# Optimization experiments

Measured on AMD Instinct MI355X. Metric: run time of the kernel, lower is better.

## Reference

```python
import jax, jax.numpy as jnp
import numpy as np

B, H, W, DIM, WS, SHIFT, HEADS = 32, 56, 56, 256, 7, 3, 8
N = WS * WS          # 49 tokens per window
C2 = 2 * DIM         # concatenated two-modal channel dim
NW = (H // WS) * (W // WS)


def _rel_index(ws):
    coords = np.stack(np.meshgrid(np.arange(ws), np.arange(ws), indexing='ij')).reshape(2, -1)
    rel = (coords[:, :, None] - coords[:, None, :]).transpose(1, 2, 0)
    rel[:, :, 0] += ws - 1
    rel[:, :, 1] += ws - 1
    rel[:, :, 0] *= 2 * ws - 1
    return rel.sum(-1)  # (N, N) int

REL_IDX = _rel_index(WS).reshape(-1)


def _attn_mask():
    # standard Swin shifted-window mask: 0 / -100 per window pair
    img = np.zeros((H, W))
    cnt = 0
    for hs in (slice(0, H - WS), slice(H - WS, H - SHIFT), slice(H - SHIFT, H)):
        for ws_ in (slice(0, W - WS), slice(W - WS, W - SHIFT), slice(W - SHIFT, W)):
            img[hs, ws_] = cnt
            cnt += 1
    mw = img.reshape(H // WS, WS, W // WS, WS).transpose(0, 2, 1, 3).reshape(-1, N)
    d = mw[:, None, :] - mw[:, :, None]
    return np.where(d != 0, -100.0, 0.0).astype(np.float32)  # (nW, N, N)

ATTN_MASK = _attn_mask()


def _win_part(x):  # (B,H,W,C) -> (nW*B, N, C)
    b, c = x.shape[0], x.shape[-1]
    x = x.reshape(b, H // WS, WS, W // WS, WS, c).transpose(0, 1, 3, 2, 4, 5)
    return x.reshape(-1, N, c)


def _win_rev(w, b):  # (nW*B, N, C) -> (B,H,W,C)
    c = w.shape[-1]
    x = w.reshape(b, H // WS, W // WS, WS, WS, c).transpose(0, 1, 3, 2, 4, 5)
    return x.reshape(b, H, W, c)


def _ln(t, g, bb):
    m = t.mean(-1, keepdims=True)
    v = t.var(-1, keepdims=True)
    return (t - m) / jnp.sqrt(v + 1e-5) * g + bb


def setup_inputs() -> dict:
    key = jax.random.key(0)
    ks = jax.random.split(key, 8)
    def nrm(k, shape, s=0.02):
        return jax.random.normal(k, shape, jnp.float32) * s
    return {
        'x': jax.random.normal(ks[0], (B, H * W, DIM), jnp.float32),
        'y': jax.random.normal(ks[1], (B, H * W, DIM), jnp.float32),
        'g1': jnp.ones((DIM,), jnp.float32), 'b1': jnp.zeros((DIM,), jnp.float32),
        'rpb': nrm(ks[2], ((2 * WS - 1) * (2 * WS - 1), HEADS)),
        'w_qkv': nrm(ks[3], (6 * DIM, 2 * DIM)), 'b_qkv': jnp.zeros((6 * DIM,), jnp.float32),
        'w_proj': nrm(ks[4], (DIM, 2 * DIM)), 'b_proj': jnp.zeros((DIM,), jnp.float32),
        'g2': jnp.ones((DIM,), jnp.float32), 'b2': jnp.zeros((DIM,), jnp.float32),
        'w_fc1': nrm(ks[5], (4 * DIM, DIM)), 'b_fc1': jnp.zeros((4 * DIM,), jnp.float32),
        'w_fc2': nrm(ks[6], (DIM, 4 * DIM)), 'b_fc2': jnp.zeros((DIM,), jnp.float32),
    }


def reference(x, y, g1, b1, rpb, w_qkv, b_qkv, w_proj, b_proj, g2, b2, w_fc1, b_fc1, w_fc2, b_fc2):
    scale = (DIM // HEADS) ** -0.5  # as in __init__: head_dim = dim // num_heads
    shortcut = x
    xn = _ln(x, g1, b1).reshape(B, H, W, DIM)
    yn = _ln(y, g1, b1).reshape(B, H, W, DIM)
    # cyclic shift
    xn = jnp.roll(xn, (-SHIFT, -SHIFT), axis=(1, 2))
    yn = jnp.roll(yn, (-SHIFT, -SHIFT), axis=(1, 2))
    xw, yw = _win_part(xn), _win_part(yn)            # (nW*B, N, C)
    xy = jnp.concatenate([xw, yw], axis=-1)          # (nW*B, N, 2C)
    nwb, hd = xy.shape[0], C2 // HEADS
    qkv = (xy @ w_qkv.T + b_qkv).reshape(nwb, N, 3, HEADS, hd).transpose(2, 0, 3, 1, 4)
    q, k, v = qkv[0] * scale, qkv[1], qkv[2]         # (nW*B, h, N, d)
    attn = jnp.einsum('whnd,whmd->whnm', q, k)
    bias = rpb[REL_IDX].reshape(N, N, HEADS).transpose(2, 0, 1)  # (h, N, N)
    attn = attn + bias[None]
    attn = attn.reshape(B, NW, HEADS, N, N) + jnp.asarray(ATTN_MASK)[None, :, None]
    attn = jax.nn.softmax(attn.reshape(nwb, HEADS, N, N), axis=-1)
    out = jnp.einsum('whnm,whmd->whnd', attn, v).transpose(0, 2, 1, 3).reshape(nwb, N, C2)
    out = out @ w_proj.T + b_proj                    # fuse 2C -> C
    out = _win_rev(out, B)
    out = jnp.roll(out, (SHIFT, SHIFT), axis=(1, 2)).reshape(B, H * W, DIM)
    x = shortcut + out
    h = _ln(x, g2, b2)
    h = jax.nn.gelu(h @ w_fc1.T + b_fc1, approximate=False)
    return x + h @ w_fc2.T + b_fc2
```

## Files before the change

kernel.cpp:

```cpp
#include <hip/hip_runtime.h>
#include <hip/hip_bf16.h>

#define DEVI __device__ __forceinline__

typedef __attribute__((ext_vector_type(8))) short short8;
typedef __attribute__((ext_vector_type(4))) float f32x4;
typedef unsigned int u32;
typedef unsigned short u16;

typedef __attribute__((address_space(1))) const u32 gu32_t;
typedef __attribute__((address_space(3))) u32 lu32_t;

DEVI u16 f2bf(float f) {
  u32 u = __builtin_bit_cast(u32, f);
  u32 r = (u + 0x7fffu + ((u >> 16) & 1u)) >> 16;
  return (u16)r;
}

DEVI f32x4 mfma16(short8 a, short8 b, f32x4 c) {
  return __builtin_amdgcn_mfma_f32_16x16x32_bf16(a, b, c, 0, 0, 0);
}

DEVI void gload16(const void* g, void* l) {
  __builtin_amdgcn_global_load_lds((gu32_t*)g, (lu32_t*)l, 16, 0, 0);
}

DEVI float gelu_s(float v) {
  return v / (1.0f + __expf(-1.702f * v));
}

#define CHUNK_ROWS 25088
#define PLANE ((size_t)CHUNK_ROWS * 64)
#define KOFF  ((size_t)8 * PLANE)
#define VOFF  ((size_t)16 * PLANE)

__global__ __launch_bounds__(256) void convall(
    const float* __restrict__ wq, const float* __restrict__ wp,
    u16* __restrict__ dq, u16* __restrict__ dp)
{
  const int i = blockIdx.x * 256 + threadIdx.x;
  const float* s; u16* d; int off;
  if (i < 196608) { s = wq; d = dq; off = i; }
  else            { s = wp; d = dp; off = i - 196608; }
  const float4 v = ((const float4*)s)[off];
  ushort4 o;
  o.x = f2bf(v.x); o.y = f2bf(v.y); o.z = f2bf(v.z); o.w = f2bf(v.w);
  ((ushort4*)d)[off] = o;
}

__global__ __launch_bounds__(256) void repack_mlp(
    const float* __restrict__ w1, const float* __restrict__ w2,
    u16* __restrict__ w1p, u16* __restrict__ w2p)
{
  const int g = blockIdx.x * 256 + threadIdx.x;
  if (g < 32768) {
    const int e0 = g * 8;
    const int chunk = e0 >> 10;
    const int colL = (e0 >> 3) & 127;
    const int kg = chunk & 3, tks = chunk >> 2;
    const int ks = tks & 7, t = tks >> 3;
    const int col = t * 128 + colL;
    const int kb = ks * 32 + kg * 8;
    short8 v;
    #pragma unroll
    for (int e = 0; e < 8; ++e) v[e] = (short)f2bf(w1[col * 256 + kb + e]);
    *(short8*)(w1p + e0) = v;
  } else {
    const int e0 = (g - 32768) * 8;
    const int chunk = e0 >> 11;
    const int outcol = (e0 >> 3) & 255;
    const int kg = chunk & 3, tks = chunk >> 2;
    const int ks = tks & 3, t = tks >> 2;
    const int kb = t * 128 + ks * 32 + kg * 8;
    short8 v;
    #pragma unroll
    for (int e = 0; e < 8; ++e) v[e] = (short)f2bf(w2[outcol * 1024 + kb + e]);
    *(short8*)(w2p + e0) = v;
  }
}

__global__ __launch_bounds__(256) void btab_build(const float* __restrict__ rpb, float* __restrict__ btab) {
  const int cls = blockIdx.x >> 3, h = blockIdx.x & 7;
  float* dst = btab + (size_t)(cls * 8 + h) * 4096;
  for (int e = threadIdx.x; e < 4096; e += 256) {
    const int q = e >> 6, l = e & 63;
    const int j = q & 3, r = (q >> 2) & 3, i = q >> 4;
    const int kg = l >> 4, rq = l & 15;
    const int n = 16 * i + kg * 4 + r;
    const int m = 16 * j + rq;
    float v;
    if (m >= 49) {
      v = -1e30f;
    } else if (n >= 49) {
      v = 0.f;
    } else {
      const int r1 = n / 7, c1 = n - r1 * 7;
      const int r2 = m / 7, c2 = m - r2 * 7;
      const int rel = (r1 - r2 + 6) * 13 + (c1 - c2 + 6);
      v = rpb[rel * 8 + h];
      const int reg1 = ((cls & 1) ? (r1 < 4 ? 1 : 2) : 0) * 3 + ((cls & 2) ? (c1 < 4 ? 1 : 2) : 0);
      const int reg2 = ((cls & 1) ? (r2 < 4 ? 1 : 2) : 0) * 3 + ((cls & 2) ? (c2 < 4 ? 1 : 2) : 0);
      if (reg1 != reg2) v -= 100.f;
    }
    dst[e] = v;
  }
}

__global__ __launch_bounds__(256) void ln_gather(
    const float* __restrict__ x, const float* __restrict__ y,
    const float* __restrict__ g1, const float* __restrict__ b1,
    u16* __restrict__ XY, int rowbase)
{
  const int wv = threadIdx.x >> 6, lane = threadIdx.x & 63;
  const int rl = blockIdx.x * 4 + wv;
  const int row = rowbase + rl;
  const int w = row / 49, n = row - w * 49;
  const int b = w >> 6, win = w & 63, wh = win >> 3, ww = win & 7;
  const int r = n / 7, c = n - r * 7;
  int oh = wh * 7 + r + 3; if (oh >= 56) oh -= 56;
  int ow = ww * 7 + c + 3; if (ow >= 56) ow -= 56;
  const size_t po = ((size_t)b * 3136 + oh * 56 + ow) * 256;
  const float4 g1v = ((const float4*)g1)[lane];
  const float4 b1v = ((const float4*)b1)[lane];
  u16* orow = XY + (size_t)rl * 512;
  #pragma unroll
  for (int mod = 0; mod < 2; ++mod) {
    const float* src = (mod ? y : x) + po;
    const float4 v = ((const float4*)src)[lane];
    float s = v.x + v.y + v.z + v.w;
    #pragma unroll
    for (int off = 1; off < 64; off <<= 1) s += __shfl_xor(s, off);
    const float mean = s * (1.0f / 256.0f);
    const float d0 = v.x - mean, d1 = v.y - mean, d2 = v.z - mean, d3 = v.w - mean;
    float sq = d0 * d0 + d1 * d1 + d2 * d2 + d3 * d3;
    #pragma unroll
    for (int off = 1; off < 64; off <<= 1) sq += __shfl_xor(sq, off);
    const float rstd = rsqrtf(sq * (1.0f / 256.0f) + 1e-5f);
    ushort4 o;
    o.x = f2bf(d0 * rstd * g1v.x + b1v.x);
    o.y = f2bf(d1 * rstd * g1v.y + b1v.y);
    o.z = f2bf(d2 * rstd * g1v.z + b1v.z);
    o.w = f2bf(d3 * rstd * g1v.w + b1v.w);
    *(ushort4*)(orow + mod * 256 + lane * 4) = o;
  }
}

__global__ __launch_bounds__(256) void qkv_gemm(
    const u16* __restrict__ A, const u16* __restrict__ Bw,
    const float* __restrict__ bias, u16* __restrict__ Qo)
{
  __shared__ __align__(16) u16 smem[128 * 128];
  u16* sA = smem;
  u16* sB = smem + 128 * 64;
  const int nx = gridDim.x;
  const int nwg = nx * gridDim.y;
  const int orig = blockIdx.y * nx + blockIdx.x;
  const int sw = (orig & 7) * (nwg >> 3) + (orig >> 3);
  const int m0  = (sw / nx) * 128;
  const int nn0 = (sw % nx) * 128;
  const int tid = threadIdx.x;
  const int lane = tid & 63;
  const int wv = tid >> 6;
  const int wm = wv >> 1, wn = wv & 1;
  const int rq = lane & 15, kg = lane >> 4;
  f32x4 acc[4][4];
  #pragma unroll
  for (int i = 0; i < 4; ++i)
    #pragma unroll
    for (int j = 0; j < 4; ++j) acc[i][j] = f32x4{0,0,0,0};

  for (int kt = 0; kt < 8; ++kt) {
    if (kt) __syncthreads();
    #pragma unroll
    for (int i = 0; i < 4; ++i) {
      const int c = i * 256 + tid;
      gload16(A + (size_t)(m0 + (c >> 3)) * 512 + kt * 64 + (c & 7) * 8, sA + c * 8);
    }
    #pragma unroll
    for (int i = 0; i < 4; ++i) {
      const int c = i * 256 + tid;
      gload16(Bw + (size_t)(nn0 + (c >> 3)) * 512 + kt * 64 + (c & 7) * 8, sB + c * 8);
    }
    __syncthreads();
    #pragma unroll
    for (int k0 = 0; k0 < 2; ++k0) {
      short8 af[4], bf8[4];
      #pragma unroll
      for (int mt = 0; mt < 4; ++mt)
        af[mt] = *(const short8*)(sA + (wm * 64 + mt * 16 + rq) * 64 + k0 * 32 + kg * 8);
      #pragma unroll
      for (int nt = 0; nt < 4; ++nt)
        bf8[nt] = *(const short8*)(sB + (wn * 64 + nt * 16 + rq) * 64 + k0 * 32 + kg * 8);
      #pragma unroll
      for (int mt = 0; mt < 4; ++mt)
        #pragma unroll
        for (int nt = 0; nt < 4; ++nt)
          acc[mt][nt] = mfma16(af[mt], bf8[nt], acc[mt][nt]);
    }
  }
  __syncthreads();
  const int t = nn0 >> 9;
  const int hbase = (nn0 & 511) >> 6;
  const float sc = (t == 0) ? 0.17677669529663687f : 1.0f;
  #pragma unroll
  for (int nt = 0; nt < 4; ++nt) {
    const int col = wn * 64 + nt * 16 + rq;
    const float bc = bias[nn0 + col];
    const int c = col >> 3;
    #pragma unroll
    for (int mt = 0; mt < 4; ++mt)
      #pragma unroll
      for (int r = 0; r < 4; ++r) {
        const int row = wm * 64 + mt * 16 + kg * 4 + r;
        smem[row * 128 + (((c & 8) | ((c ^ row) & 7)) << 3) + (col & 7)] =
            f2bf((acc[mt][nt][r] + bc) * sc);
      }
  }
  __syncthreads();
  #pragma unroll
  for (int it = 0; it < 8; ++it) {
    const int idx = it * 256 + tid;
    const int hh = idx >> 10;
    const int c8 = (idx >> 7) & 7;
    const int rowL = idx & 127;
    const int c = hh * 8 + c8;
    const int grow = m0 + rowL;
    const u32 w49 = (u32)grow / 49u;
    const u32 tok = (u32)grow - w49 * 49u;
    const short8 v = *(const short8*)(smem + rowL * 128 + (((c & 8) | ((c ^ rowL) & 7)) << 3));
    *(short8*)(Qo + (size_t)(t * 8 + hbase + hh) * PLANE + (size_t)w49 * 3136 + (c8 * 49 + tok) * 8) = v;
  }
}

__global__ __launch_bounds__(128, 3) void attn3(
    const u16* __restrict__ qkv, const float* __restrict__ btab,
    u16* __restrict__ concat, int wbase)
{
  __shared__ __align__(16) u16 sP[2][3136];
  __shared__ __align__(16) u16 sVT[2][4608];

  const int tid = threadIdx.x;
  const int wv = tid >> 6, lane = tid & 63;
  const int rq = lane & 15, kg = lane >> 4;
  const int gw = blockIdx.x * 2 + wv;
  const int wl = gw >> 3, h = gw & 7;
  const int w = wbase + wl;
  const int win = w & 63, wh = win >> 3, ww = win & 7;
  const int cls = ((wh == 7) ? 1 : 0) | ((ww == 7) ? 2 : 0);
  const float* Tb = btab + (size_t)(cls * 8 + h) * 4096;
  u16* sPw = sP[wv];
  u16* sVw = sVT[wv];

  const u16* qbase = qkv + (size_t)h * PLANE + (size_t)wl * 3136;
  const u16* kbase = qkv + KOFF + (size_t)h * PLANE + (size_t)wl * 3136;
  const u16* vbase = qkv + VOFF + (size_t)h * PLANE + (size_t)wl * 3136;

  short8 vreg[4][2];
  #pragma unroll
  for (int t = 0; t < 4; ++t) {
    const int tokc = (16 * t + rq) > 48 ? 48 : (16 * t + rq);
    #pragma unroll
    for (int h2 = 0; h2 < 2; ++h2)
      vreg[t][h2] = *(const short8*)(vbase + ((h2 * 4 + kg) * 49 + tokc) * 8);
  }

  short8 ak[4][2];
  #pragma unroll
  for (int j = 0; j < 4; ++j) {
    const int rr = (16 * j + rq) > 48 ? 48 : (16 * j + rq);
    ak[j][0] = *(const short8*)(kbase + (kg * 49 + rr) * 8);
    ak[j][1] = *(const short8*)(kbase + ((4 + kg) * 49 + rr) * 8);
  }
  f32x4 sacc[4][4];
  #pragma unroll
  for (int i = 0; i < 4; ++i)
    #pragma unroll
    for (int j = 0; j < 4; ++j) sacc[i][j] = f32x4{0,0,0,0};
  #pragma unroll
  for (int i = 0; i < 4; ++i) {
    const int rr = (16 * i + rq) > 48 ? 48 : (16 * i + rq);
    const short8 a0 = *(const short8*)(qbase + (kg * 49 + rr) * 8);
    const short8 a1 = *(const short8*)(qbase + ((4 + kg) * 49 + rr) * 8);
    #pragma unroll
    for (int j = 0; j < 4; ++j) {
      sacc[i][j] = mfma16(a0, ak[j][0], sacc[i][j]);
      sacc[i][j] = mfma16(a1, ak[j][1], sacc[i][j]);
    }
  }

  #pragma unroll
  for (int t = 0; t < 4; ++t) {
    const int row = 16 * t + rq;
    #pragma unroll
    for (int h2 = 0; h2 < 2; ++h2) {
      const int c0 = kg * 8 + h2 * 32;
      #pragma unroll
      for (int j = 0; j < 8; ++j)
        sVw[(c0 + j) * 72 + (row ^ (kg << 4))] = (u16)vreg[t][h2][j];
    }
  }

  #pragma unroll
  for (int i = 0; i < 4; ++i) {
    #pragma unroll
    for (int r = 0; r < 4; ++r) {
      const int n = 16 * i + kg * 4 + r;
      const float* Tq = Tb + ((i * 4 + r) * 4) * 64 + lane;
      float pv[4];
      #pragma unroll
      for (int j = 0; j < 4; ++j)
        pv[j] = sacc[i][j][r] + Tq[j * 64];
      float mx = fmaxf(fmaxf(pv[0], pv[1]), fmaxf(pv[2], pv[3]));
      #pragma unroll
      for (int off = 1; off < 16; off <<= 1) mx = fmaxf(mx, __shfl_xor(mx, off));
      float sm = 0.f;
      #pragma unroll
      for (int j = 0; j < 4; ++j) { const float e = __expf(pv[j] - mx); pv[j] = e; sm += e; }
      #pragma unroll
      for (int off = 1; off < 16; off <<= 1) sm += __shfl_xor(sm, off);
      const float inv = 1.0f / sm;
      if (n < 49) {
        #pragma unroll
        for (int j = 0; j < 4; ++j) {
          const int col = 16 * j + rq;
          sPw[n * 64 + (((col >> 3) ^ (n & 7)) << 3) + (col & 7)] = f2bf(pv[j] * inv);
        }
      }
    }
  }

  f32x4 oacc[4][4];
  #pragma unroll
  for (int i = 0; i < 4; ++i)
    #pragma unroll
    for (int j = 0; j < 4; ++j) oacc[i][j] = f32x4{0,0,0,0};
  #pragma unroll
  for (int m0v = 0; m0v < 2; ++m0v) {
    short8 av[4];
    #pragma unroll
    for (int ct = 0; ct < 4; ++ct) {
      const int col = ct * 16 + rq;
      const int s = (col >> 3) & 3;
      short8 vvv = *(const short8*)(sVw + col * 72 + ((m0v * 32 + kg * 8) ^ (s << 4)));
      if (m0v == 1) {
        if (kg == 3) {
          #pragma unroll
          for (int e = 0; e < 8; ++e) vvv[e] = 0;
        } else if (kg == 2) {
          #pragma unroll
          for (int e = 1; e < 8; ++e) vvv[e] = 0;
        }
      }
      av[ct] = vvv;
    }
    #pragma unroll
    for (int i = 0; i < 4; ++i) {
      const int rr = (16 * i + rq) > 48 ? 48 : (16 * i + rq);
      const int ch = (m0v * 4 + kg) ^ (rr & 7);
      const short8 pa = *(const short8*)(sPw + rr * 64 + ch * 8);
      #pragma unroll
      for (int ct = 0; ct < 4; ++ct)
        oacc[i][ct] = mfma16(pa, av[ct], oacc[i][ct]);
    }
  }

  __builtin_amdgcn_s_waitcnt(0);
  #pragma unroll
  for (int i = 0; i < 4; ++i)
    #pragma unroll
    for (int ct = 0; ct < 4; ++ct)
      #pragma unroll
      for (int r = 0; r < 4; ++r) {
        const int n = 16 * i + kg * 4 + r;
        if (n < 49) {
          const int col = ct * 16 + rq;
          sPw[n * 64 + (((col >> 3) ^ (n & 7)) << 3) + (col & 7)] = f2bf(oacc[i][ct][r]);
        }
      }
  u16* crow = concat + (size_t)(wl * 49) * 512 + h * 64;
  #pragma unroll
  for (int it = 0; it < 7; ++it) {
    const int c = it * 64 + lane;
    if (c < 392) {
      const int m = c >> 3, s = c & 7;
      const short8 vvv = *(const short8*)(sPw + m * 64 + ((s ^ (m & 7)) << 3));
      *(short8*)(crow + (size_t)m * 512 + s * 8) = vvv;
    }
  }
}

__global__ __launch_bounds__(256, 3) void projln(
    const u16* __restrict__ A, const u16* __restrict__ Bw,
    const float* __restrict__ bias, const float* __restrict__ x,
    const float* __restrict__ g2, const float* __restrict__ b2,
    float* __restrict__ out, u16* __restrict__ xn2, int rowbase)
{
  __shared__ __align__(16) u16 sA[64 * 64];
  __shared__ __align__(16) u16 sB[256 * 64];
  const int m0 = blockIdx.x * 64;
  const int tid = threadIdx.x;
  const int lane = tid & 63;
  const int wv = tid >> 6;
  const int rq = lane & 15, kg = lane >> 4;
  f32x4 acc[16];
  #pragma unroll
  for (int j = 0; j < 16; ++j) acc[j] = f32x4{0,0,0,0};

  for (int kt = 0; kt < 8; ++kt) {
    if (kt) __syncthreads();
    #pragma unroll
    for (int i = 0; i < 2; ++i) {
      const int c = i * 256 + tid;
      gload16(A + (size_t)(m0 + (c >> 3)) * 512 + kt * 64 + (c & 7) * 8, sA + c * 8);
    }
    #pragma unroll
    for (int i = 0; i < 8; ++i) {
      const int c = i * 256 + tid;
      gload16(Bw + (size_t)(c >> 3) * 512 + kt * 64 + (c & 7) * 8, sB + c * 8);
    }
    __syncthreads();
    #pragma unroll
    for (int k0 = 0; k0 < 2; ++k0) {
      const short8 af = *(const short8*)(sA + (wv * 16 + rq) * 64 + k0 * 32 + kg * 8);
      #pragma unroll
      for (int nt = 0; nt < 16; ++nt) {
        const short8 bf8 = *(const short8*)(sB + (nt * 16 + rq) * 64 + k0 * 32 + kg * 8);
        acc[nt] = mfma16(af, bf8, acc[nt]);
      }
    }
  }

  float br[16], g2r[16], b2r[16];
  #pragma unroll
  for (int nt = 0; nt < 16; ++nt) {
    const int col = nt * 16 + rq;
    br[nt] = bias[col]; g2r[nt] = g2[col]; b2r[nt] = b2[col];
  }
  #pragma unroll
  for (int r = 0; r < 4; ++r) {
    const int row = m0 + wv * 16 + kg * 4 + r;
    const u32 g = (u32)(rowbase + row);
    const u32 w = g / 49u; const u32 n = g - w * 49u;
    const int b = w >> 6, win = w & 63, wh = win >> 3, ww = win & 7;
    const u32 rr = n / 7u; const u32 cc = n - rr * 7u;
    int oh = wh * 7 + (int)rr + 3; if (oh >= 56) oh -= 56;
    int ow = ww * 7 + (int)cc + 3; if (ow >= 56) ow -= 56;
    const size_t po = ((size_t)b * 3136 + oh * 56 + ow) * 256;
    float vals[16];
    float s = 0.f;
    #pragma unroll
    for (int nt = 0; nt < 16; ++nt) {
      const float v = acc[nt][r] + br[nt] + x[po + nt * 16 + rq];
      vals[nt] = v; s += v;
    }
    #pragma unroll
    for (int off = 1; off < 16; off <<= 1) s += __shfl_xor(s, off);
    const float mean = s * (1.0f / 256.0f);
    float sq = 0.f;
    #pragma unroll
    for (int nt = 0; nt < 16; ++nt) { const float d_ = vals[nt] - mean; sq += d_ * d_; }
    #pragma unroll
    for (int off = 1; off < 16; off <<= 1) sq += __shfl_xor(sq, off);
    const float rstd = rsqrtf(sq * (1.0f / 256.0f) + 1e-5f);
    #pragma unroll
    for (int nt = 0; nt < 16; ++nt) {
      const int col = nt * 16 + rq;
      out[po + col] = vals[nt];
      xn2[po + col] = f2bf((vals[nt] - mean) * rstd * g2r[nt] + b2r[nt]);
    }
  }
}

__global__ __launch_bounds__(256, 3) void fused_mlp(
    const u16* __restrict__ xn2, const u16* __restrict__ w1p,
    const float* __restrict__ bf1, const u16* __restrict__ w2p,
    const float* __restrict__ bf2v, float* __restrict__ out)
{
  __shared__ __align__(16) u16 sX[64 * 256];
  __shared__ __align__(16) u16 sH[64 * 128];

  const int m0 = blockIdx.x * 64;
  const int tid = threadIdx.x;
  const int wv = tid >> 6, lane = tid & 63;
  const int rq = lane & 15, kg = lane >> 4;

  #pragma unroll
  for (int i = 0; i < 8; ++i) {
    const int c = i * 256 + tid;
    const int row = c >> 5, ch = c & 31;
    const int sch = (ch & 24) | ((ch ^ row) & 7);
    gload16(xn2 + (size_t)(m0 + row) * 256 + sch * 8, sX + c * 8);
  }

  f32x4 acc2[4][4];
  #pragma unroll
  for (int i = 0; i < 4; ++i)
    #pragma unroll
    for (int j = 0; j < 4; ++j) acc2[i][j] = f32x4{0,0,0,0};

  __syncthreads();

  for (int t = 0; t < 8; ++t) {
    f32x4 a1[4][2];
    #pragma unroll
    for (int i = 0; i < 4; ++i)
      #pragma unroll
      for (int j = 0; j < 2; ++j) a1[i][j] = f32x4{0,0,0,0};
    #pragma unroll
    for (int ks = 0; ks < 8; ++ks) {
      const u16* wb = w1p + ((size_t)((t * 8 + ks) * 4 + kg)) * 1024;
      short8 bfr[2];
      #pragma unroll
      for (int nt = 0; nt < 2; ++nt)
        bfr[nt] = *(const short8*)(wb + (wv * 32 + nt * 16 + rq) * 8);
      #pragma unroll
      for (int mt = 0; mt < 4; ++mt) {
        const int R = mt * 16 + rq;
        const int wk = ks * 4 + kg;
        const short8 af = *(const short8*)(sX + R * 256 + ((wk & 24) | ((wk ^ R) & 7)) * 8);
        #pragma unroll
        for (int nt = 0; nt < 2; ++nt)
          a1[mt][nt] = mfma16(af, bfr[nt], a1[mt][nt]);
      }
    }
    __syncthreads();
    #pragma unroll
    for (int nt = 0; nt < 2; ++nt) {
      const int col = wv * 32 + nt * 16 + rq;
      const float bb = bf1[t * 128 + col];
      const int ch = col >> 3;
      #pragma unroll
      for (int mt = 0; mt < 4; ++mt)
        #pragma unroll
        for (int r = 0; r < 4; ++r) {
          const int row = mt * 16 + kg * 4 + r;
          sH[row * 128 + ((ch & 8) | ((ch ^ row) & 7)) * 8 + (col & 7)] =
              f2bf(gelu_s(a1[mt][nt][r] + bb));
        }
    }
    __syncthreads();
    #pragma unroll
    for (int ks = 0; ks < 4; ++ks) {
      const u16* wb = w2p + ((size_t)((t * 4 + ks) * 4 + kg)) * 2048;
      short8 bfr2[4];
      #pragma unroll
      for (int nt = 0; nt < 4; ++nt)
        bfr2[nt] = *(const short8*)(wb + (wv * 64 + nt * 16 + rq) * 8);
      #pragma unroll
      for (int mt = 0; mt < 4; ++mt) {
        const int R = mt * 16 + rq;
        const int wk = ks * 4 + kg;
        const short8 af = *(const short8*)(sH + R * 128 + ((wk & 8) | ((wk ^ R) & 7)) * 8);
        #pragma unroll
        for (int nt = 0; nt < 4; ++nt)
          acc2[mt][nt] = mfma16(af, bfr2[nt], acc2[mt][nt]);
      }
    }
  }

  #pragma unroll
  for (int nt = 0; nt < 4; ++nt) {
    const int col = wv * 64 + nt * 16 + rq;
    const float bb = bf2v[col];
    #pragma unroll
    for (int mt = 0; mt < 4; ++mt)
      #pragma unroll
      for (int r = 0; r < 4; ++r) {
        float* p = out + (size_t)(m0 + mt * 16 + kg * 4 + r) * 256 + col;
        *p = acc2[mt][nt][r] + bb + *p;
      }
  }
}

extern "C" void kernel_launch(void* const* d_in, const int* in_sizes, int n_in,
                              void* d_out, int out_size, void* d_ws, size_t ws_size,
                              hipStream_t stream) {
  const float* x      = (const float*)d_in[0];
  const float* y      = (const float*)d_in[1];
  const float* g1     = (const float*)d_in[2];
  const float* b1     = (const float*)d_in[3];
  const float* rpb    = (const float*)d_in[4];
  const float* w_qkv  = (const float*)d_in[5];
  const float* b_qkv  = (const float*)d_in[6];
  const float* w_proj = (const float*)d_in[7];
  const float* b_proj = (const float*)d_in[8];
  const float* g2     = (const float*)d_in[9];
  const float* b2     = (const float*)d_in[10];
  const float* w_fc1  = (const float*)d_in[11];
  const float* b_fc1  = (const float*)d_in[12];
  const float* w_fc2  = (const float*)d_in[13];
  const float* b_fc2  = (const float*)d_in[14];
  float* out = (float*)d_out;

  u16* wsp = (u16*)d_ws;
  u16* wqkv_bf  = wsp;
  u16* wproj_bf = wsp + 786432;
  u16* w1p      = wsp + 917504;
  u16* w2p      = wsp + 1179648;
  float* btab   = (float*)(wsp + 1441792);
  u16* xn2      = wsp + 1703936;
  u16* XYc      = wsp + 27394048;
  u16* qkvc     = wsp + 40239104;

  convall<<<896, 256, 0, stream>>>(w_qkv, w_proj, wqkv_bf, wproj_bf);
  repack_mlp<<<256, 256, 0, stream>>>(w_fc1, w_fc2, w1p, w2p);
  btab_build<<<32, 256, 0, stream>>>(rpb, btab);

  for (int c = 0; c < 4; ++c) {
    ln_gather<<<6272, 256, 0, stream>>>(x, y, g1, b1, XYc, c * CHUNK_ROWS);
    qkv_gemm<<<dim3(12, 196), 256, 0, stream>>>(XYc, wqkv_bf, b_qkv, qkvc);
    attn3<<<2048, 128, 0, stream>>>(qkvc, btab, XYc, c * 512);
    projln<<<392, 256, 0, stream>>>(XYc, wproj_bf, b_proj, x, g2, b2, out, xn2, c * CHUNK_ROWS);
  }

  fused_mlp<<<1568, 256, 0, stream>>>(xn2, w1p, b_fc1, w2p, b_fc2, out);
}
```

Baseline: 793.7 us.

## Software-pipeline MLP fc1 of next chunk with fc2 of current chunk

Restructures the fused MLP kernel so the fc1 GEMM for hidden chunk t+1 is interleaved with the fc2 GEMM for chunk t, with the first fc1 chunk hoisted before the loop. This gives the scheduler independent MFMA chains and global weight loads to overlap, hiding load latency. It also raises wave priority around the MFMA section. The cost is extra accumulator registers (a1n), which may raise register pressure and lower occupancy.

```diff
diff --git a/kernel.cpp b/kernel.cpp
--- a/kernel.cpp
+++ b/kernel.cpp
@@ -500,29 +500,30 @@
 
   __syncthreads();
 
+  f32x4 a1[4][2];
+  #pragma unroll
+  for (int i = 0; i < 4; ++i)
+    #pragma unroll
+    for (int j = 0; j < 2; ++j) a1[i][j] = f32x4{0,0,0,0};
+  #pragma unroll
+  for (int ks = 0; ks < 8; ++ks) {
+    const u16* wb = w1p + ((size_t)(ks * 4 + kg)) * 1024;
+    short8 bfr[2];
+    #pragma unroll
+    for (int nt = 0; nt < 2; ++nt)
+      bfr[nt] = *(const short8*)(wb + (wv * 32 + nt * 16 + rq) * 8);
+    #pragma unroll
+    for (int mt = 0; mt < 4; ++mt) {
+      const int R = mt * 16 + rq;
+      const int wk = ks * 4 + kg;
+      const short8 af = *(const short8*)(sX + R * 256 + ((wk & 24) | ((wk ^ R) & 7)) * 8);
+      #pragma unroll
+      for (int nt = 0; nt < 2; ++nt)
+        a1[mt][nt] = mfma16(af, bfr[nt], a1[mt][nt]);
+    }
+  }
+
   for (int t = 0; t < 8; ++t) {
-    f32x4 a1[4][2];
-    #pragma unroll
-    for (int i = 0; i < 4; ++i)
-      #pragma unroll
-      for (int j = 0; j < 2; ++j) a1[i][j] = f32x4{0,0,0,0};
-    #pragma unroll
-    for (int ks = 0; ks < 8; ++ks) {
-      const u16* wb = w1p + ((size_t)((t * 8 + ks) * 4 + kg)) * 1024;
-      short8 bfr[2];
-      #pragma unroll
-      for (int nt = 0; nt < 2; ++nt)
-        bfr[nt] = *(const short8*)(wb + (wv * 32 + nt * 16 + rq) * 8);
-      #pragma unroll
-      for (int mt = 0; mt < 4; ++mt) {
-        const int R = mt * 16 + rq;
-        const int wk = ks * 4 + kg;
-        const short8 af = *(const short8*)(sX + R * 256 + ((wk & 24) | ((wk ^ R) & 7)) * 8);
-        #pragma unroll
-        for (int nt = 0; nt < 2; ++nt)
-          a1[mt][nt] = mfma16(af, bfr[nt], a1[mt][nt]);
-      }
-    }
     __syncthreads();
     #pragma unroll
     for (int nt = 0; nt < 2; ++nt) {
@@ -539,23 +540,74 @@
         }
     }
     __syncthreads();
-    #pragma unroll
-    for (int ks = 0; ks < 4; ++ks) {
-      const u16* wb = w2p + ((size_t)((t * 4 + ks) * 4 + kg)) * 2048;
-      short8 bfr2[4];
-      #pragma unroll
-      for (int nt = 0; nt < 4; ++nt)
-        bfr2[nt] = *(const short8*)(wb + (wv * 64 + nt * 16 + rq) * 8);
-      #pragma unroll
-      for (int mt = 0; mt < 4; ++mt) {
-        const int R = mt * 16 + rq;
-        const int wk = ks * 4 + kg;
-        const short8 af = *(const short8*)(sH + R * 128 + ((wk & 8) | ((wk ^ R) & 7)) * 8);
+    __builtin_amdgcn_s_setprio(1);
+    if (t < 7) {
+      f32x4 a1n[4][2];
+      #pragma unroll
+      for (int i = 0; i < 4; ++i)
+        #pragma unroll
+        for (int j = 0; j < 2; ++j) a1n[i][j] = f32x4{0,0,0,0};
+      #pragma unroll
+      for (int ks2 = 0; ks2 < 4; ++ks2) {
+        {
+          const u16* wb2 = w2p + ((size_t)((t * 4 + ks2) * 4 + kg)) * 2048;
+          short8 bfr2[4];
+          #pragma unroll
+          for (int nt = 0; nt < 4; ++nt)
+            bfr2[nt] = *(const short8*)(wb2 + (wv * 64 + nt * 16 + rq) * 8);
+          #pragma unroll
+          for (int mt = 0; mt < 4; ++mt) {
+            const int R = mt * 16 + rq;
+            const int wk = ks2 * 4 + kg;
+            const short8 af = *(const short8*)(sH + R * 128 + ((wk & 8) | ((wk ^ R) & 7)) * 8);
+            #pragma unroll
+            for (int nt = 0; nt < 4; ++nt)
+              acc2[mt][nt] = mfma16(af, bfr2[nt], acc2[mt][nt]);
+          }
+        }
+        #pragma unroll
+        for (int s = 0; s < 2; ++s) {
+          const int ks = ks2 * 2 + s;
+          const u16* wb = w1p + ((size_t)(((t + 1) * 8 + ks) * 4 + kg)) * 1024;
+          short8 bfr[2];
+          #pragma unroll
+          for (int nt = 0; nt < 2; ++nt)
+            bfr[nt] = *(const short8*)(wb + (wv * 32 + nt * 16 + rq) * 8);
+          #pragma unroll
+          for (int mt = 0; mt < 4; ++mt) {
+            const int R = mt * 16 + rq;
+            const int wk = ks * 4 + kg;
+            const short8 af = *(const short8*)(sX + R * 256 + ((wk & 24) | ((wk ^ R) & 7)) * 8);
+            #pragma unroll
+            for (int nt = 0; nt < 2; ++nt)
+              a1n[mt][nt] = mfma16(af, bfr[nt], a1n[mt][nt]);
+          }
+        }
+      }
+      #pragma unroll
+      for (int i = 0; i < 4; ++i)
+        #pragma unroll
+        for (int j = 0; j < 2; ++j) a1[i][j] = a1n[i][j];
+    } else {
+      #pragma unroll
+      for (int ks2 = 0; ks2 < 4; ++ks2) {
+        const u16* wb2 = w2p + ((size_t)((t * 4 + ks2) * 4 + kg)) * 2048;
+        short8 bfr2[4];
         #pragma unroll
         for (int nt = 0; nt < 4; ++nt)
-          acc2[mt][nt] = mfma16(af, bfr2[nt], acc2[mt][nt]);
-      }
-    }
+          bfr2[nt] = *(const short8*)(wb2 + (wv * 64 + nt * 16 + rq) * 8);
+        #pragma unroll
+        for (int mt = 0; mt < 4; ++mt) {
+          const int R = mt * 16 + rq;
+          const int wk = ks2 * 4 + kg;
+          const short8 af = *(const short8*)(sH + R * 128 + ((wk & 8) | ((wk ^ R) & 7)) * 8);
+          #pragma unroll
+          for (int nt = 0; nt < 4; ++nt)
+            acc2[mt][nt] = mfma16(af, bfr2[nt], acc2[mt][nt]);
+        }
+      }
+    }
+    __builtin_amdgcn_s_setprio(0);
   }
 
   #pragma unroll
```

Measured after the change: 1.189 ms. +49.8%, slower.
